# Kernel optimization log

Measured on AMD Instinct MI355X. Metric: run time of the kernel, lower is better.

The kernel has to match this reference:

```python
import jax, jax.numpy as jnp
import numpy as np
import math

P = 2
TAU = 1.0
USE_POW = False
ALIGN_W = 1.0
ENTROPY_W = 1.0
EPS = 1e-12


def _pairwise_l2(z):
    # torch.cdist(z, z, p=2): sqrt of squared distances via GEMM decomposition
    sq = jnp.sum(z * z, axis=-1)  # [N]
    d2 = sq[:, None] + sq[None, :] - 2.0 * (z @ z.T)  # [N, N]
    d = jnp.sqrt(jnp.maximum(d2, 0.0))
    return jnp.maximum(d, EPS)  # clamp_min(eps)


def setup_inputs() -> dict:
    key = jax.random.key(0)
    k0, k1 = jax.random.split(key)
    v0 = jax.random.normal(k0, (8192, 256), dtype=jnp.float32)
    v1 = jax.random.normal(k1, (8192, 256), dtype=jnp.float32)
    return {"v0": v0, "v1": v1}


def reference(v0, v1):
    views = [v0, v1]
    n = v0.shape[0]

    # Alignment term: mean Lp distance between matched rows, one pair (0,1)
    diff = v0 - v1
    align = jnp.sqrt(jnp.sum(diff * diff, axis=-1)).mean()  # p=2 norm per row

    # Entropy term: masked logsumexp over within-view pairwise distances
    log_num_neg = math.log(n - 1)
    eye = jnp.eye(n, dtype=bool)
    entropy = jnp.float32(0.0)
    for z in views:
        dist = _pairwise_l2(z)  # [N, N]
        logits = jnp.where(eye, -jnp.inf, -dist / TAU)
        lme = jax.nn.logsumexp(logits, axis=1) - log_num_neg  # [N]
        entropy = entropy + lme.mean()
    entropy = entropy / len(views)

    return ALIGN_W * align + ENTROPY_W * entropy
```

## Files before the change

kernel.cpp:

```cpp
#include <hip/hip_runtime.h>
#include <math.h>


#define D_DIM 256
#define NB 64
#define NBLK 2080
#define S_Q 26.0f
#define LOG2E2 2.0813689810f

typedef int i32x4 __attribute__((ext_vector_type(4)));
typedef unsigned int u32;
#define AS1 __attribute__((address_space(1)))
#define AS3 __attribute__((address_space(3)))

__device__ inline void load_lds16(const void* g, void* l) {
  __builtin_amdgcn_global_load_lds((const AS1 u32*)g, (AS3 u32*)l, 16, 0, 0);
}

__device__ inline int q8(float x) {
  return __float2int_rn(fminf(fmaxf(x * S_Q, -127.0f), 127.0f));
}
__device__ inline u32 q8x4(const float4 f) {
  return (u32)(q8(f.x) & 255) | ((u32)(q8(f.y) & 255) << 8) |
         ((u32)(q8(f.z) & 255) << 16) | ((u32)(q8(f.w) & 255) << 24);
}

__global__ __launch_bounds__(256) void prep(
    const float* __restrict__ v0, const float* __restrict__ v1,
    unsigned char* __restrict__ ph0, unsigned char* __restrict__ ph1,
    float* __restrict__ sq0, float* __restrict__ sq1,
    float* __restrict__ S0, float* __restrict__ S1,
    float* __restrict__ align_part) {
  __shared__ float4 l0[1024], l1[1024];
  __shared__ float red0[4][16], red1[4][16], red2[4][16];
  const int R = blockIdx.x;
  const int t = threadIdx.x;

  #pragma unroll
  for (int p = 0; p < 4; ++p) {
    const int slot = t + p * 256;
    const size_t g = (size_t)(R * 16 + (slot >> 6)) * 64 + (slot & 63);
    l0[slot] = ((const float4*)v0)[g];
    l1[slot] = ((const float4*)v1)[g];
  }
  __syncthreads();

  {
    const int rr = t & 15, c = t >> 4;
    const int s = c >> 2, q = c & 3;
    const int li = rr * 64 + c * 4;
    uint4 u0, u1;
    u0.x = q8x4(l0[li + 0]); u0.y = q8x4(l0[li + 1]);
    u0.z = q8x4(l0[li + 2]); u0.w = q8x4(l0[li + 3]);
    u1.x = q8x4(l1[li + 0]); u1.y = q8x4(l1[li + 1]);
    u1.z = q8x4(l1[li + 2]); u1.w = q8x4(l1[li + 3]);
    const size_t dst = (size_t)(R * 4 + s) * 64 + q * 16 + rr;
    ((uint4*)ph0)[dst] = u0;
    ((uint4*)ph1)[dst] = u1;
  }

  {
    const int rr = t & 15;
    const int base = rr * 64 + (t >> 4) * 4;
    float s0p = 0.f, s1p = 0.f, s2p = 0.f;
    #pragma unroll
    for (int c = 0; c < 4; ++c) {
      const float4 a = l0[base + c], b = l1[base + c];
      s0p += a.x * a.x + a.y * a.y + a.z * a.z + a.w * a.w;
      s1p += b.x * b.x + b.y * b.y + b.z * b.z + b.w * b.w;
      const float dx = a.x - b.x, dy = a.y - b.y, dz = a.z - b.z, dw = a.w - b.w;
      s2p += dx * dx + dy * dy + dz * dz + dw * dw;
    }
    s0p += __shfl_xor(s0p, 16, 64); s0p += __shfl_xor(s0p, 32, 64);
    s1p += __shfl_xor(s1p, 16, 64); s1p += __shfl_xor(s1p, 32, 64);
    s2p += __shfl_xor(s2p, 16, 64); s2p += __shfl_xor(s2p, 32, 64);
    const int w = t >> 6, lane = t & 63;
    if (lane < 16) { red0[w][lane] = s0p; red1[w][lane] = s1p; red2[w][lane] = s2p; }
  }
  __syncthreads();
  if (t < 16) {
    const int row = R * 16 + t;
    const float a0 = red0[0][t] + red0[1][t] + red0[2][t] + red0[3][t];
    const float a1 = red1[0][t] + red1[1][t] + red1[2][t] + red1[3][t];
    const float a2 = red2[0][t] + red2[1][t] + red2[2][t] + red2[3][t];
    sq0[row] = a0 * LOG2E2;
    sq1[row] = a1 * LOG2E2;
    align_part[row] = sqrtf(a2);
    S0[row] = 0.0f;
    S1[row] = 0.0f;
  }
}

__global__ __launch_bounds__(256) void entropy_tile(
    const unsigned char* __restrict__ ph0, const unsigned char* __restrict__ ph1,
    const float* __restrict__ sq0, const float* __restrict__ sq1,
    float* __restrict__ S0, float* __restrict__ S1) {
  const unsigned char* __restrict__ ph = blockIdx.y ? ph1 : ph0;
  const float* __restrict__ sq = blockIdx.y ? sq1 : sq0;
  float* __restrict__ S        = blockIdx.y ? S1 : S0;

  const int b = blockIdx.x;
  int bi = (int)((129.0 - sqrt(16641.0 - 8.0 * (double)b)) * 0.5);
  while ((bi + 1) * NB - ((bi + 1) * bi) / 2 <= b) ++bi;
  while (bi * NB - (bi * (bi - 1)) / 2 > b) --bi;
  const int bj = bi + (b - (bi * NB - (bi * (bi - 1)) / 2));
  const bool diag = (bi == bj);

  __shared__ __align__(16) char smem[32768];
  float* swp = (float*)smem;

  const int t = threadIdx.x, lane = t & 63, w = t >> 6;
  const int wi = w >> 1, wj = w & 1;
  const int quad = lane >> 4, l15 = lane & 15;
  const int i0 = bi * 128, j0 = bj * 128;

  #pragma unroll
  for (int r8 = 0; r8 < 8; ++r8) {
    const int seg = w * 8 + r8;
    const unsigned char* src = ph + (size_t)bi * 32768 + seg * 1024 + lane * 16;
    load_lds16(src, smem + seg * 1024);
  }

  const i32x4* __restrict__ phv = (const i32x4*)ph;
  const int baseB = ((bj * 8 + wj * 4) * 4) * 64 + lane;

  i32x4 bF[2][4];
  #pragma unroll
  for (int n = 0; n < 4; ++n) bF[0][n] = phv[baseB + (n * 4) * 64];

  i32x4 acc[4][4];
  #pragma unroll
  for (int m = 0; m < 4; ++m)
    #pragma unroll
    for (int n = 0; n < 4; ++n)
      acc[m][n] = (i32x4){0, 0, 0, 0};

  __syncthreads();

  const i32x4* smemv = (const i32x4*)smem;
  #pragma unroll
  for (int s = 0; s < 4; ++s) {
    const int cur = s & 1, nxt = cur ^ 1;
    if (s < 3) {
      #pragma unroll
      for (int n = 0; n < 4; ++n)
        bF[nxt][n] = phv[baseB + (n * 4 + s + 1) * 64];
    }
    i32x4 ah[4];
    #pragma unroll
    for (int m = 0; m < 4; ++m)
      ah[m] = smemv[(size_t)((wi * 4 + m) * 4 + s) * 64 + lane];
    #pragma unroll
    for (int m = 0; m < 4; ++m)
      #pragma unroll
      for (int n = 0; n < 4; ++n)
        acc[m][n] = __builtin_amdgcn_mfma_i32_16x16x64_i8(ah[m], bF[cur][n], acc[m][n], 0, 0, 0);
  }

  __syncthreads();

  const float K2 = 2.0f * LOG2E2 / (S_Q * S_Q);
  float sj[4];
  #pragma unroll
  for (int n = 0; n < 4; ++n) sj[n] = sq[j0 + wj * 64 + n * 16 + l15];

  const int wbase = w * 1088;
  float csum[4] = {0.f, 0.f, 0.f, 0.f};
  #pragma unroll
  for (int m = 0; m < 4; ++m) {
    #pragma unroll
    for (int r = 0; r < 4; ++r) {
      const int rowl = m * 16 + quad * 4 + r;
      const int gi = i0 + wi * 64 + rowl;
      const float si = sq[gi];
      float p = 0.f;
      #pragma unroll
      for (int n = 0; n < 4; ++n) {
        const float d2 = fmaxf(fmaf(-K2, (float)acc[m][n][r], si + sj[n]), 0.0f);
        const float dist = __builtin_amdgcn_sqrtf(d2);
        float e = __builtin_amdgcn_exp2f(-dist);
        if (diag && gi == j0 + wj * 64 + n * 16 + l15) e = 0.f;
        p += e;
        csum[n] += e;
      }
      swp[wbase + rowl * 17 + l15] = p;
    }
  }
  {
    float rs = 0.f;
    #pragma unroll
    for (int j = 0; j < 16; ++j) rs += swp[wbase + lane * 17 + j];
    atomicAdd(&S[i0 + wi * 64 + lane], rs);
  }
  if (!diag) {
    #pragma unroll
    for (int n = 0; n < 4; ++n) {
      float c2 = csum[n];
      c2 += __shfl_xor(c2, 16, 64);
      c2 += __shfl_xor(c2, 32, 64);
      if (quad == 0) atomicAdd(&S[j0 + wj * 64 + n * 16 + l15], c2);
    }
  }
}

__global__ __launch_bounds__(256) void finalize_part(
    const float* __restrict__ S0, const float* __restrict__ S1,
    const float* __restrict__ align_part,
    float* __restrict__ part_log, float* __restrict__ part_align) {
  __shared__ float shl[4], sha[4];
  const int t = threadIdx.x, lane = t & 63, w = t >> 6;
  const int idx = blockIdx.x * 256 + t;
  float lg = __logf(S0[idx]) + __logf(S1[idx]);
  float al = align_part[idx];
  #pragma unroll
  for (int o = 1; o < 64; o <<= 1) {
    lg += __shfl_xor(lg, o, 64);
    al += __shfl_xor(al, o, 64);
  }
  if (lane == 0) { shl[w] = lg; sha[w] = al; }
  __syncthreads();
  if (t == 0) {
    part_log[blockIdx.x] = shl[0] + shl[1] + shl[2] + shl[3];
    part_align[blockIdx.x] = sha[0] + sha[1] + sha[2] + sha[3];
  }
}

__global__ void finalize_final(const float* __restrict__ part_log,
                               const float* __restrict__ part_align,
                               float* __restrict__ out, int n) {
  const int lane = threadIdx.x & 63;
  double lg = (lane < 32) ? (double)part_log[lane] : 0.0;
  double al = (lane < 32) ? (double)part_align[lane] : 0.0;
  #pragma unroll
  for (int o = 1; o < 32; o <<= 1) {
    lg += __shfl_xor(lg, o, 64);
    al += __shfl_xor(al, o, 64);
  }
  if (lane == 0) {
    double align = al / (double)n;
    double entropy = 0.5 * lg / (double)n - log((double)(n - 1));
    out[0] = (float)(align + entropy);
  }
}

extern "C" void kernel_launch(void* const* d_in, const int* in_sizes, int n_in,
                              void* d_out, int out_size, void* d_ws, size_t ws_size,
                              hipStream_t stream) {
  const float* v0 = (const float*)d_in[0];
  const float* v1 = (const float*)d_in[1];
  float* out = (float*)d_out;
  const int n = in_sizes[0] / D_DIM;

  float* ws         = (float*)d_ws;
  float* sq0        = ws;
  float* sq1        = ws + n;
  float* S0         = ws + 2 * n;
  float* S1         = ws + 3 * n;
  float* align_part = ws + 4 * n;
  float* part_log   = ws + 5 * n;
  float* part_align = ws + 5 * n + 32;
  unsigned char* ph0 = (unsigned char*)(ws + 5 * n + 64);
  unsigned char* ph1 = ph0 + (size_t)n * D_DIM;

  prep<<<n / 16, 256, 0, stream>>>(v0, v1, ph0, ph1, sq0, sq1, S0, S1, align_part);

  dim3 grid(NBLK, 2);
  entropy_tile<<<grid, 256, 0, stream>>>(ph0, ph1, sq0, sq1, S0, S1);

  finalize_part<<<n / 256, 256, 0, stream>>>(S0, S1, align_part, part_log, part_align);
  finalize_final<<<1, 64, 0, stream>>>(part_log, part_align, out, n);
}
```

Measured before the change: 120.2 us.

## Fuse finalize into entropy tile via last-block counter and split diagonal epilogue

Removes the two finalize kernel launches by having the last entropy_tile block, found through an atomic counter reset in prep, reduce the logs and alignment and write the output. The epilogue is split into diagonal and off-diagonal paths, so off-diagonal tiles skip the self-pair mask compare. It also drops the fmax clamp before sqrt and hoists the sj loads ahead of the MFMA loop. In exchange it adds a threadfence and a global atomic per block, and the final reduction runs serially in one block. Without the clamp, a slightly negative d2 from rounding could give NaN on near-duplicate rows.

Measured after the change: 349.2 us. 190% more time.

```diff
diff --git a/kernel.cpp b/kernel.cpp
--- a/kernel.cpp
+++ b/kernel.cpp
@@ -30,11 +30,13 @@
     unsigned char* __restrict__ ph0, unsigned char* __restrict__ ph1,
     float* __restrict__ sq0, float* __restrict__ sq1,
     float* __restrict__ S0, float* __restrict__ S1,
-    float* __restrict__ align_part) {
+    float* __restrict__ align_part, int* __restrict__ cnt) {
   __shared__ float4 l0[1024], l1[1024];
   __shared__ float red0[4][16], red1[4][16], red2[4][16];
   const int R = blockIdx.x;
   const int t = threadIdx.x;
+
+  if (R == 0 && t == 0) *cnt = 0;
 
   #pragma unroll
   for (int p = 0; p < 4; ++p) {
@@ -94,7 +96,9 @@
 __global__ __launch_bounds__(256) void entropy_tile(
     const unsigned char* __restrict__ ph0, const unsigned char* __restrict__ ph1,
     const float* __restrict__ sq0, const float* __restrict__ sq1,
-    float* __restrict__ S0, float* __restrict__ S1) {
+    float* __restrict__ S0, float* __restrict__ S1,
+    const float* __restrict__ align_part, int* __restrict__ cnt,
+    float* __restrict__ out, int nrows) {
   const unsigned char* __restrict__ ph = blockIdx.y ? ph1 : ph0;
   const float* __restrict__ sq = blockIdx.y ? sq1 : sq0;
   float* __restrict__ S        = blockIdx.y ? S1 : S0;
@@ -135,6 +139,10 @@
     for (int n = 0; n < 4; ++n)
       acc[m][n] = (i32x4){0, 0, 0, 0};
 
+  float sj[4];
+  #pragma unroll
+  for (int n = 0; n < 4; ++n) sj[n] = sq[j0 + wj * 64 + n * 16 + l15];
+
   __syncthreads();
 
   const i32x4* smemv = (const i32x4*)smem;
@@ -160,39 +168,31 @@
   __syncthreads();
 
   const float K2 = 2.0f * LOG2E2 / (S_Q * S_Q);
-  float sj[4];
-  #pragma unroll
-  for (int n = 0; n < 4; ++n) sj[n] = sq[j0 + wj * 64 + n * 16 + l15];
-
   const int wbase = w * 1088;
-  float csum[4] = {0.f, 0.f, 0.f, 0.f};
-  #pragma unroll
-  for (int m = 0; m < 4; ++m) {
-    #pragma unroll
-    for (int r = 0; r < 4; ++r) {
-      const int rowl = m * 16 + quad * 4 + r;
-      const int gi = i0 + wi * 64 + rowl;
-      const float si = sq[gi];
-      float p = 0.f;
-      #pragma unroll
-      for (int n = 0; n < 4; ++n) {
-        const float d2 = fmaxf(fmaf(-K2, (float)acc[m][n][r], si + sj[n]), 0.0f);
-        const float dist = __builtin_amdgcn_sqrtf(d2);
-        float e = __builtin_amdgcn_exp2f(-dist);
-        if (diag && gi == j0 + wj * 64 + n * 16 + l15) e = 0.f;
-        p += e;
-        csum[n] += e;
+
+  if (!diag) {
+    float csum[4] = {0.f, 0.f, 0.f, 0.f};
+    #pragma unroll
+    for (int m = 0; m < 4; ++m) {
+      #pragma unroll
+      for (int r = 0; r < 4; ++r) {
+        const int rowl = m * 16 + quad * 4 + r;
+        const float si = sq[i0 + wi * 64 + rowl];
+        float p = 0.f;
+        #pragma unroll
+        for (int n = 0; n < 4; ++n) {
+          const float d2 = fmaf(-K2, (float)acc[m][n][r], si + sj[n]);
+          const float e = __builtin_amdgcn_exp2f(-__builtin_amdgcn_sqrtf(d2));
+          p += e;
+          csum[n] += e;
+        }
+        swp[wbase + rowl * 17 + l15] = p;
       }
-      swp[wbase + rowl * 17 + l15] = p;
-    }
-  }
-  {
+    }
     float rs = 0.f;
     #pragma unroll
     for (int j = 0; j < 16; ++j) rs += swp[wbase + lane * 17 + j];
     atomicAdd(&S[i0 + wi * 64 + lane], rs);
-  }
-  if (!diag) {
     #pragma unroll
     for (int n = 0; n < 4; ++n) {
       float c2 = csum[n];
@@ -200,46 +200,54 @@
       c2 += __shfl_xor(c2, 32, 64);
       if (quad == 0) atomicAdd(&S[j0 + wj * 64 + n * 16 + l15], c2);
     }
-  }
-}
-
-__global__ __launch_bounds__(256) void finalize_part(
-    const float* __restrict__ S0, const float* __restrict__ S1,
-    const float* __restrict__ align_part,
-    float* __restrict__ part_log, float* __restrict__ part_align) {
-  __shared__ float shl[4], sha[4];
-  const int t = threadIdx.x, lane = t & 63, w = t >> 6;
-  const int idx = blockIdx.x * 256 + t;
-  float lg = __logf(S0[idx]) + __logf(S1[idx]);
-  float al = align_part[idx];
-  #pragma unroll
-  for (int o = 1; o < 64; o <<= 1) {
-    lg += __shfl_xor(lg, o, 64);
-    al += __shfl_xor(al, o, 64);
-  }
-  if (lane == 0) { shl[w] = lg; sha[w] = al; }
-  __syncthreads();
-  if (t == 0) {
-    part_log[blockIdx.x] = shl[0] + shl[1] + shl[2] + shl[3];
-    part_align[blockIdx.x] = sha[0] + sha[1] + sha[2] + sha[3];
-  }
-}
-
-__global__ void finalize_final(const float* __restrict__ part_log,
-                               const float* __restrict__ part_align,
-                               float* __restrict__ out, int n) {
-  const int lane = threadIdx.x & 63;
-  double lg = (lane < 32) ? (double)part_log[lane] : 0.0;
-  double al = (lane < 32) ? (double)part_align[lane] : 0.0;
-  #pragma unroll
-  for (int o = 1; o < 32; o <<= 1) {
-    lg += __shfl_xor(lg, o, 64);
-    al += __shfl_xor(al, o, 64);
-  }
-  if (lane == 0) {
-    double align = al / (double)n;
-    double entropy = 0.5 * lg / (double)n - log((double)(n - 1));
-    out[0] = (float)(align + entropy);
+  } else {
+    #pragma unroll
+    for (int m = 0; m < 4; ++m) {
+      #pragma unroll
+      for (int r = 0; r < 4; ++r) {
+        const int rowl = m * 16 + quad * 4 + r;
+        const int gi = i0 + wi * 64 + rowl;
+        const float si = sq[gi];
+        float p = 0.f;
+        #pragma unroll
+        for (int n = 0; n < 4; ++n) {
+          const float d2 = fmaf(-K2, (float)acc[m][n][r], si + sj[n]);
+          float e = __builtin_amdgcn_exp2f(-__builtin_amdgcn_sqrtf(d2));
+          if (gi == j0 + wj * 64 + n * 16 + l15) e = 0.f;
+          p += e;
+        }
+        swp[wbase + rowl * 17 + l15] = p;
+      }
+    }
+    float rs = 0.f;
+    #pragma unroll
+    for (int j = 0; j < 16; ++j) rs += swp[wbase + lane * 17 + j];
+    atomicAdd(&S[i0 + wi * 64 + lane], rs);
+  }
+
+  __threadfence();
+  int* isLast = (int*)(smem + 17408);
+  if (t == 0) *isLast = (atomicAdd(cnt, 1) == 2 * NBLK - 1);
+  __syncthreads();
+  if (*isLast) {
+    double lg = 0.0, al = 0.0;
+    for (int i = t; i < nrows; i += 256) {
+      lg += (double)__logf(S0[i]) + (double)__logf(S1[i]);
+      al += (double)align_part[i];
+    }
+    double* dsh = (double*)(smem + 17424);
+    dsh[t] = lg;
+    dsh[256 + t] = al;
+    __syncthreads();
+    for (int off = 128; off > 0; off >>= 1) {
+      if (t < off) { dsh[t] += dsh[t + off]; dsh[256 + t] += dsh[256 + t + off]; }
+      __syncthreads();
+    }
+    if (t == 0) {
+      const double align = dsh[256] / (double)nrows;
+      const double entropy = 0.5 * dsh[0] / (double)nrows - log((double)(nrows - 1));
+      out[0] = (float)(align + entropy);
+    }
   }
 }
 
@@ -257,16 +265,13 @@
   float* S0         = ws + 2 * n;
   float* S1         = ws + 3 * n;
   float* align_part = ws + 4 * n;
-  float* part_log   = ws + 5 * n;
-  float* part_align = ws + 5 * n + 32;
+  int*   cnt        = (int*)(ws + 5 * n);
   unsigned char* ph0 = (unsigned char*)(ws + 5 * n + 64);
   unsigned char* ph1 = ph0 + (size_t)n * D_DIM;
 
-  prep<<<n / 16, 256, 0, stream>>>(v0, v1, ph0, ph1, sq0, sq1, S0, S1, align_part);
+  prep<<<n / 16, 256, 0, stream>>>(v0, v1, ph0, ph1, sq0, sq1, S0, S1, align_part, cnt);
 
   dim3 grid(NBLK, 2);
-  entropy_tile<<<grid, 256, 0, stream>>>(ph0, ph1, sq0, sq1, S0, S1);
-
-  finalize_part<<<n / 256, 256, 0, stream>>>(S0, S1, align_part, part_log, part_align);
-  finalize_final<<<1, 64, 0, stream>>>(part_log, part_align, out, n);
-}
+  entropy_tile<<<grid, 256, 0, stream>>>(ph0, ph1, sq0, sq1, S0, S1,
+                                         align_part, cnt, out, n);
+}
```
